# Performance work log

Hardware: AMD Instinct MI355X
Metric: run time of the kernel (lower is better)

The kernel has to match this reference:

```python
import jax, jax.numpy as jnp
import numpy as np
import math

L_, E_, H_, F_ = 6, 256, 8, 2048
NQ, B_, M_ = 300, 8, 1024

def _lin(x, w, b):
    return x @ w.T + b

def _ln(x, w, b):
    m = jnp.mean(x, -1, keepdims=True)
    v = jnp.var(x, -1, keepdims=True)
    return (x - m) / jnp.sqrt(v + 1e-5) * w + b

def _mha(q, k, v, iw, ib, ow, ob, H):
    # torch nn.MultiheadAttention, seq-first [L, B, E], packed in_proj
    E = q.shape[-1]; Dh = E // H
    wq, wk, wv = iw[:E], iw[E:2*E], iw[2*E:]
    bq, bk, bv = ib[:E], ib[E:2*E], ib[2*E:]
    qp = (_lin(q, wq, bq) * (Dh ** -0.5)).reshape(q.shape[0], q.shape[1], H, Dh)
    kp = _lin(k, wk, bk).reshape(k.shape[0], k.shape[1], H, Dh)
    vp = _lin(v, wv, bv).reshape(v.shape[0], v.shape[1], H, Dh)
    att = jax.nn.softmax(jnp.einsum('qbhd,kbhd->bhqk', qp, kp), axis=-1)
    o = jnp.einsum('bhqk,kbhd->qbhd', att, vp).reshape(q.shape[0], q.shape[1], E)
    return _lin(o, ow, ob)

def _sine4(pt):
    # pt: [nq, b, 4]; faithful to gen_sineembed_for_position4 incl. the
    # pos_w/pos_h re-use of the already-transformed pos_x/pos_y (original bug).
    dim_t = 10000.0 ** (2 * (jnp.arange(64) // 2).astype(jnp.float32) / 64)
    s = 2 * math.pi
    def iv(p):
        return jnp.stack([jnp.sin(p[:, :, 0::2]), jnp.cos(p[:, :, 1::2])], axis=3).reshape(p.shape[0], p.shape[1], -1)
    px = iv(pt[:, :, 0, None] * s / dim_t)
    py = iv(pt[:, :, 1, None] * s / dim_t)
    pw = iv(px)
    ph = iv(py)
    return jnp.concatenate([py, px, pw, ph], axis=2)


def setup_inputs() -> dict:
    key = jax.random.key(0)
    ks = iter(jax.random.split(key, 80))
    rn = lambda *s: jax.random.normal(next(ks), s, dtype=jnp.float32)
    rw = lambda *s: jax.random.normal(next(ks), s, dtype=jnp.float32) * 0.02
    d = dict(
        tgt=rn(NQ, B_, E_), memory=rn(M_, B_, E_), pos=rn(M_, B_, E_),
        query_pos=rn(NQ, B_, E_), box_embed=rn(NQ, B_, 4),
        sa_in_w=rw(L_, 3*E_, E_), sa_in_b=rw(L_, 3*E_), sa_out_w=rw(L_, E_, E_), sa_out_b=rw(L_, E_),
        ca_in_w=rw(L_, 3*E_, E_), ca_in_b=rw(L_, 3*E_), ca_out_w=rw(L_, E_, E_), ca_out_b=rw(L_, E_),
        ca_qpos_w=rw(E_, E_), ca_qpos_b=rw(E_),
        ca_kpos_w=rw(L_, E_, E_), ca_kpos_b=rw(L_, E_),
        ca_v_w=rw(L_, E_, E_), ca_v_b=rw(L_, E_),
        ca_kc_w=rw(L_, E_, E_), ca_kc_b=rw(L_, E_),
        ca_qs_w=rw(L_, E_, E_), ca_qs_b=rw(L_, E_),
        ca_vp_w=rw(L_, E_, E_), ca_vp_b=rw(L_, E_),
        lin1_w=rw(L_, F_, E_), lin1_b=rw(L_, F_), lin2_w=rw(L_, E_, F_), lin2_b=rw(L_, E_),
        lp1_w=rw(L_, F_, E_), lp1_b=rw(L_, F_), lp2_w=rw(L_, E_, F_), lp2_b=rw(L_, E_),
        norms_w=jnp.ones((L_, 6, E_), jnp.float32), norms_b=jnp.zeros((L_, 6, E_), jnp.float32),
        qs_w1=rw(E_, E_), qs_b1=rw(E_), qs_w2=rw(E_, E_), qs_b2=rw(E_),
        rh_w1=rw(E_, E_), rh_b1=rw(E_), rh_w2=rw(4, E_), rh_b2=rw(4),
        bo_w1=rw(L_, E_ // 2, 4), bo_b1=rw(L_, E_ // 2), bo_w2=rw(L_, 4, E_ // 2), bo_b2=rw(L_, 4),
    )
    return d


def _fwd(tgt, memory, pos, query_pos, box_embed, sa_in_w, sa_in_b, sa_out_w, sa_out_b,
         ca_in_w, ca_in_b, ca_out_w, ca_out_b, ca_qpos_w, ca_qpos_b, ca_kpos_w, ca_kpos_b,
         ca_v_w, ca_v_b, ca_kc_w, ca_kc_b, ca_qs_w, ca_qs_b, ca_vp_w, ca_vp_b,
         lin1_w, lin1_b, lin2_w, lin2_b, lp1_w, lp1_b, lp2_w, lp2_b, norms_w, norms_b,
         qs_w1, qs_b1, qs_w2, qs_b2, rh_w1, rh_b1, rh_w2, rh_b2, bo_w1, bo_b1, bo_w2, bo_b2):
    H = H_
    L = sa_in_w.shape[0]
    relu = jax.nn.relu
    # ref_point_head: MLP(d, d, 4, 2)
    rbs = _lin(relu(_lin(query_pos, rh_w1, rh_b1)), rh_w2, rh_b2)  # [nq,b,4]
    out = tgt
    for l in range(L):
        pt = 1.0 if l == 0 else _lin(relu(_lin(out, qs_w1, qs_b1)), qs_w2, qs_b2)
        rbs = rbs + _lin(relu(_lin(box_embed, bo_w1[l], bo_b1[l])), bo_w2[l], bo_b2[l])
        qse = _sine4(jax.nn.sigmoid(rbs)) * pt  # [nq,b,256]
        # self-attention (q = k = out + query_pos, v = out)
        q = out + query_pos
        t = _ln(out + _mha(q, q, out, sa_in_w[l], sa_in_b[l], sa_out_w[l], sa_out_b[l], H),
                norms_w[l, 0], norms_b[l, 0])
        # conditional cross-attention projections
        if l == 0:
            qc = t + _lin(query_pos, ca_qpos_w, ca_qpos_b)
            kk = memory + pos; v = memory; kpos = pos
        else:
            qc = t
            kpos = _lin(pos, ca_kpos_w[l], ca_kpos_b[l])
            v = _lin(memory, ca_v_w[l], ca_v_b[l])
            kk = _lin(memory, ca_kc_w[l], ca_kc_b[l])
        qse_p = _lin(qse, ca_qs_w[l], ca_qs_b[l])
        t2 = _mha(qc, kk, v, ca_in_w[l], ca_in_b[l], ca_out_w[l], ca_out_b[l], H)
        vpos = _lin(memory, ca_vp_w[l], ca_vp_b[l])
        t2p = _mha(qse_p, kpos, vpos, ca_in_w[l], ca_in_b[l], ca_out_w[l], ca_out_b[l], H)
        t2 = t2 + t2p
        # positional branch FFN
        tp = _ln(t + t2p, norms_w[l, 3], norms_b[l, 3])
        tp = _ln(tp + _lin(relu(_lin(tp, lp1_w[l], lp1_b[l])), lp2_w[l], lp2_b[l]),
                 norms_w[l, 4], norms_b[l, 4])
        # main branch FFN
        t = _ln(t + t2, norms_w[l, 1], norms_b[l, 1])
        t = _ln(t + _lin(relu(_lin(t, lin1_w[l], lin1_b[l])), lin2_w[l], lin2_b[l]),
                norms_w[l, 2], norms_b[l, 2])
        out = _ln(t + tp, norms_w[l, 5], norms_b[l, 5])
    return out[None]  # [1, nq, b, d] (return_intermediate=False -> unsqueeze(0))


def reference(tgt, memory, pos, query_pos, box_embed, sa_in_w, sa_in_b, sa_out_w, sa_out_b,
              ca_in_w, ca_in_b, ca_out_w, ca_out_b, ca_qpos_w, ca_qpos_b, ca_kpos_w, ca_kpos_b,
              ca_v_w, ca_v_b, ca_kc_w, ca_kc_b, ca_qs_w, ca_qs_b, ca_vp_w, ca_vp_b,
              lin1_w, lin1_b, lin2_w, lin2_b, lp1_w, lp1_b, lp2_w, lp2_b, norms_w, norms_b,
              qs_w1, qs_b1, qs_w2, qs_b2, rh_w1, rh_b1, rh_w2, rh_b2, bo_w1, bo_b1, bo_w2, bo_b2):
    return _fwd(tgt, memory, pos, query_pos, box_embed, sa_in_w, sa_in_b, sa_out_w, sa_out_b,
                ca_in_w, ca_in_b, ca_out_w, ca_out_b, ca_qpos_w, ca_qpos_b, ca_kpos_w, ca_kpos_b,
                ca_v_w, ca_v_b, ca_kc_w, ca_kc_b, ca_qs_w, ca_qs_b, ca_vp_w, ca_vp_b,
                lin1_w, lin1_b, lin2_w, lin2_b, lp1_w, lp1_b, lp2_w, lp2_b, norms_w, norms_b,
                qs_w1, qs_b1, qs_w2, qs_b2, rh_w1, rh_b1, rh_w2, rh_b2, bo_w1, bo_b1, bo_w2, bo_b2)
```

## Files before the change

### kernel.cpp

```cpp
#include <hip/hip_runtime.h>
#include <hip/hip_bf16.h>

#define NQq 300
#define BBb 8
#define MMm 1024
#define EEe 256
#define FFf 2048
#define LLl 6
#define RQ 2400
#define RM 8192
#define RPAD 2432

typedef unsigned short u16;
typedef short bf16x8 __attribute__((ext_vector_type(8)));
typedef float f32x4 __attribute__((ext_vector_type(4)));

__device__ __forceinline__ float u2f(u16 u){ return __uint_as_float(((unsigned)u)<<16); }
__device__ __forceinline__ u16 f2u(float v){
  __hip_bfloat16 h = __float2bfloat16(v);
  return *reinterpret_cast<u16*>(&h);
}
__device__ __forceinline__ int effdt(int t, int f){ return (t==0) ? 1 : ((t==1) ? 0 : (f?1:0)); }
__device__ __forceinline__ float ldd(const void* p, size_t i, int t, int f){
  if (t == 0) return ((const float*)p)[i];
  if (t == 1) return u2f(((const u16*)p)[i]);
  return f ? ((const float*)p)[i] : u2f(((const u16*)p)[i]);
}
__device__ __forceinline__ void ld8f(const void* p, size_t eoff, int e, float* o){
  if (e == 0) {
    uint4 v = *(const uint4*)((const u16*)p + eoff);
    u16 tmp[8]; *(uint4*)tmp = v;
#pragma unroll
    for (int u = 0; u < 8; ++u) o[u] = u2f(tmp[u]);
  } else {
    const float* q = (const float*)p + eoff;
    float4 v0 = ((const float4*)q)[0], v1 = ((const float4*)q)[1];
    o[0]=v0.x;o[1]=v0.y;o[2]=v0.z;o[3]=v0.w;o[4]=v1.x;o[5]=v1.y;o[6]=v1.z;o[7]=v1.w;
  }
}
__device__ __forceinline__ uint4 ld8pack(const void* p, size_t eoff, int e){
  if (e == 0) return *(const uint4*)((const u16*)p + eoff);
  float o[8]; ld8f(p, eoff, 1, o);
  u16 tmp[8];
#pragma unroll
  for (int u = 0; u < 8; ++u) tmp[u] = f2u(o[u]);
  return *(uint4*)tmp;
}

__global__ void k_flag_init(int* flag){ if (threadIdx.x==0 && blockIdx.x==0) *flag = 0; }
__global__ void k_detect(const u16* __restrict__ p, int n, int* flag){
  int hit = 0;
  for (int i = blockIdx.x*blockDim.x + threadIdx.x; i < n; i += gridDim.x*blockDim.x){
    u16 u = p[i];
    if ((u & 0x7F80u) == 0x7F80u) hit = 1;
  }
  if (hit) atomicOr(flag, 1);
}

__global__ void k_cvt_in(const void* __restrict__ s, float* __restrict__ d, int n,
                         const int* __restrict__ flag){
  int f = *flag;
  for (int i = blockIdx.x*blockDim.x + threadIdx.x; i < n; i += gridDim.x*blockDim.x)
    d[i] = ldd(s, i, 2, f);
}
__global__ void k_out_dual(const float* __restrict__ s, void* __restrict__ d, int n,
                           const int* __restrict__ flag){
  int f = *flag;
  for (int i = blockIdx.x*blockDim.x + threadIdx.x; i < n; i += gridDim.x*blockDim.x){
    if (f) ((float*)d)[i] = s[i];
    else   ((u16*)d)[i] = f2u(s[i]);
  }
}

struct CompW { const void* A[27]; size_t ao[27]; const void* B[27]; size_t bo[27]; u16* W[27]; };
__global__ __launch_bounds__(256) void k_compose_w(CompW cw, const int* __restrict__ flag){
  int f = *flag;
  int z = blockIdx.z;
  const void* A = cw.A[z]; size_t ao = cw.ao[z];
  const void* B = cw.B[z]; size_t bo = cw.bo[z];
  u16* Wo = cw.W[z];
  int ea = effdt(2,f), eb = ea;
  __shared__ __align__(16) u16 As[64*40];
  __shared__ __align__(16) u16 Bs[64*40];
  int bm = blockIdx.x*64, bn = blockIdx.y*64;
  int t = threadIdx.x;
  int lane = t & 63, wv = t >> 6;
  int wrow = (wv>>1)<<5, wcol = (wv&1)<<5;
  int quad = lane>>4, mr = lane&15;
  f32x4 a00 = {0.f,0.f,0.f,0.f}, a01 = a00, a10 = a00, a11 = a00;
  for (int k0 = 0; k0 < 256; k0 += 32){
    { int srow = t>>2, scg = (t&3)<<3;
      *(uint4*)&As[srow*40+scg] = ld8pack(A, ao + (size_t)(bm+srow)*256 + k0 + scg, ea); }
    { int kk = t>>3, c8 = (t&7)<<3;
      float o8[8]; ld8f(B, bo + (size_t)(k0+kk)*256 + bn + c8, eb, o8);
#pragma unroll
      for (int u = 0; u < 8; ++u) Bs[(c8+u)*40 + kk] = f2u(o8[u]); }
    __syncthreads();
    bf16x8 a0 = *(const bf16x8*)&As[(wrow+mr)*40+quad*8];
    bf16x8 a1 = *(const bf16x8*)&As[(wrow+16+mr)*40+quad*8];
    bf16x8 b0 = *(const bf16x8*)&Bs[(wcol+mr)*40+quad*8];
    bf16x8 b1 = *(const bf16x8*)&Bs[(wcol+16+mr)*40+quad*8];
    a00 = __builtin_amdgcn_mfma_f32_16x16x32_bf16(a0,b0,a00,0,0,0);
    a01 = __builtin_amdgcn_mfma_f32_16x16x32_bf16(a0,b1,a01,0,0,0);
    a10 = __builtin_amdgcn_mfma_f32_16x16x32_bf16(a1,b0,a10,0,0,0);
    a11 = __builtin_amdgcn_mfma_f32_16x16x32_bf16(a1,b1,a11,0,0,0);
    __syncthreads();
  }
  f32x4 av[4] = {a00,a01,a10,a11};
#pragma unroll
  for (int i = 0; i < 2; ++i)
#pragma unroll
  for (int j = 0; j < 2; ++j){
    f32x4 a = av[i*2+j];
    int col = bn + wcol + j*16 + mr;
#pragma unroll
    for (int r = 0; r < 4; ++r){
      int row = bm + wrow + i*16 + quad*4 + r;
      Wo[(size_t)row*256 + col] = f2u(a[r]);
    }
  }
}
struct CompB { const void* A[27]; size_t ao[27]; const void* b1[27]; size_t b1o[27];
               const void* b2[27]; size_t b2o[27]; u16* bo[27]; };
__global__ __launch_bounds__(256) void k_compose_b(CompB cb, const int* __restrict__ flag){
  int f = *flag;
  int z = blockIdx.x, o = threadIdx.x;
  float acc = 0.f;
  for (int j = 0; j < 256; ++j)
    acc += ldd(cb.A[z], cb.ao[z] + (size_t)o*256 + j, 2, f) * ldd(cb.b1[z], cb.b1o[z] + j, 2, f);
  cb.bo[z][o] = f2u(acc + ldd(cb.b2[z], cb.b2o[z] + o, 2, f));
}

__global__ __launch_bounds__(256) void k_gemm(
    const void* __restrict__ X1, size_t xo1, int xt1,
    const void* __restrict__ X2, size_t xo2, int xt2,
    const void* __restrict__ W1, size_t wo1, int wt1,
    const void* __restrict__ B1v, size_t bo1, int bt1,
    const void* __restrict__ W2, size_t wo2, int wt2,
    const void* __restrict__ B2v, size_t bo2, int bt2,
    void* __restrict__ Y, int yt, int ldy,
    int R, int K, int O, int Rsplit, int relu, const int* __restrict__ flag)
{
  __shared__ __align__(16) u16 As[64*40];
  __shared__ __align__(16) u16 Bs[64*40];
  int f = *flag;
  int bm = blockIdx.x*64, bn = blockIdx.y*64;
  bool second = (bm >= Rsplit);
  const void* W = second ? W2 : W1;  size_t wo = second ? wo2 : wo1;  int wt = second ? wt2 : wt1;
  const void* Bv = second ? B2v : B1v; size_t bo = second ? bo2 : bo1; int bt = second ? bt2 : bt1;
  int ex1 = effdt(xt1, f), ew = effdt(wt, f);
  int t = threadIdx.x;
  int srow = t >> 2, scg = (t & 3) << 3;
  int lane = t & 63, wv = t >> 6;
  int wrow = (wv >> 1) << 5, wcol = (wv & 1) << 5;
  int quad = lane >> 4, mr = lane & 15;
  f32x4 acc00 = {0.f,0.f,0.f,0.f}, acc01 = acc00, acc10 = acc00, acc11 = acc00;
  for (int k0 = 0; k0 < K; k0 += 32) {
    {
      int gr = bm + srow;
      uint4 v = {0u,0u,0u,0u};
      if (gr < R) {
        size_t e = xo1 + (size_t)gr*K + k0 + scg;
        if (xt2 < 0) v = ld8pack(X1, e, ex1);
        else {
          float a8[8], b8[8];
          ld8f(X1, e, ex1, a8);
          ld8f(X2, xo2 + (size_t)gr*K + k0 + scg, effdt(xt2,f), b8);
          u16 tmp[8];
#pragma unroll
          for (int u = 0; u < 8; ++u) tmp[u] = f2u(a8[u] + b8[u]);
          v = *(uint4*)tmp;
        }
      }
      *(uint4*)&As[srow*40 + scg] = v;
    }
    {
      int go = bn + srow;
      uint4 v = {0u,0u,0u,0u};
      if (go < O) v = ld8pack(W, wo + (size_t)go*K + k0 + scg, ew);
      *(uint4*)&Bs[srow*40 + scg] = v;
    }
    __syncthreads();
    bf16x8 a0 = *(const bf16x8*)&As[(wrow      + mr)*40 + quad*8];
    bf16x8 a1 = *(const bf16x8*)&As[(wrow + 16 + mr)*40 + quad*8];
    bf16x8 b0 = *(const bf16x8*)&Bs[(wcol      + mr)*40 + quad*8];
    bf16x8 b1 = *(const bf16x8*)&Bs[(wcol + 16 + mr)*40 + quad*8];
    acc00 = __builtin_amdgcn_mfma_f32_16x16x32_bf16(a0, b0, acc00, 0, 0, 0);
    acc01 = __builtin_amdgcn_mfma_f32_16x16x32_bf16(a0, b1, acc01, 0, 0, 0);
    acc10 = __builtin_amdgcn_mfma_f32_16x16x32_bf16(a1, b0, acc10, 0, 0, 0);
    acc11 = __builtin_amdgcn_mfma_f32_16x16x32_bf16(a1, b1, acc11, 0, 0, 0);
    __syncthreads();
  }
  f32x4 av[4] = {acc00, acc01, acc10, acc11};
#pragma unroll
  for (int i = 0; i < 2; ++i)
#pragma unroll
  for (int j = 0; j < 2; ++j) {
    f32x4 a = av[i*2 + j];
    int col = bn + wcol + j*16 + mr;
    if (col >= O) continue;
    float bv = ldd(Bv, bo + col, bt, f);
#pragma unroll
    for (int r = 0; r < 4; ++r) {
      int row = bm + wrow + i*16 + quad*4 + r;
      if (row >= R) continue;
      float v = a[r] + bv;
      if (relu) v = fmaxf(v, 0.f);
      if (yt == 0) ((float*)Y)[(size_t)row*ldy + col] = v;
      else         ((u16*)Y)[(size_t)row*ldy + col] = f2u(v);
    }
  }
}

__device__ __forceinline__ float blk_sum256(float v, float* red){
  for (int off = 32; off; off >>= 1) v += __shfl_down(v, off, 64);
  int lane = threadIdx.x & 63, w = threadIdx.x >> 6;
  if (lane == 0) red[w] = v;
  __syncthreads();
  v = red[0] + red[1] + red[2] + red[3];
  __syncthreads();
  return v;
}
__device__ __forceinline__ float ln_one(float x, size_t go, size_t bo,
    const void* gb, const void* bb, int f, float* red, int i){
  float m = blk_sum256(x, red) * (1.0f/256.0f);
  float d0 = x - m;
  float var = blk_sum256(d0*d0, red) * (1.0f/256.0f);
  float r = rsqrtf(var + 1e-5f);
  return d0 * r * ldd(gb, go + i, 2, f) + ldd(bb, bo + i, 2, f);
}
__global__ __launch_bounds__(256) void k_ln(
    const float* __restrict__ A, const float* __restrict__ Bp, const float* __restrict__ Cp,
    const void* __restrict__ gb, const void* __restrict__ bb, size_t o1,
    float* __restrict__ Y, const int* __restrict__ flag)
{
  __shared__ float red[4];
  int f = *flag;
  int row = blockIdx.x, i = threadIdx.x;
  size_t idx = (size_t)row*256 + i;
  float x = A[idx];
  if (Bp) x += Bp[idx];
  if (Cp) x += Cp[idx];
  Y[idx] = ln_one(x, o1, o1, gb, bb, f, red, i);
}
__global__ __launch_bounds__(256) void k_ln_pair(
    const float* __restrict__ A1, const float* __restrict__ B1, const float* __restrict__ C1,
    size_t o1, float* __restrict__ Y1,
    const float* __restrict__ A2, const float* __restrict__ B2,
    size_t o2, float* __restrict__ Y2,
    const void* __restrict__ gb, const void* __restrict__ bb, const int* __restrict__ flag)
{
  __shared__ float red[4];
  int f = *flag;
  int row = blockIdx.x, i = threadIdx.x;
  size_t idx = (size_t)row*256 + i;
  float x1 = A1[idx] + B1[idx];
  if (C1) x1 += C1[idx];
  float x2 = A2[idx] + B2[idx];
  float y1 = ln_one(x1, o1, o1, gb, bb, f, red, i);
  float y2 = ln_one(x2, o2, o2, gb, bb, f, red, i);
  Y1[idx] = y1;
  Y2[idx] = y2;
}

struct FP {
  const u16* Q[2]; int qs[2];
  const u16* K[2]; int ks[2];
  const u16* V[2]; int vs[2];
  u16* O[2];
};
__global__ __launch_bounds__(256) void k_flash_pair(FP fp, int NQr, int Nk, float scale)
{
  __shared__ __align__(16) u16 Qs[64*40];
  __shared__ __align__(16) u16 Ks[64*40];
  __shared__ __align__(16) u16 Vs[32*72];
  __shared__ __align__(16) u16 Ps[64*72];
  int z = blockIdx.z;
  const u16* Q = fp.Q[z]; int qstr = fp.qs[z];
  const u16* K = fp.K[z]; int kstr = fp.ks[z];
  const u16* V = fp.V[z]; int vstr = fp.vs[z];
  u16* O = fp.O[z];
  int t = threadIdx.x;
  int b = blockIdx.y >> 3, h = blockIdx.y & 7;
  int q0 = blockIdx.x * 64;
  int lane = t & 63, wv = t >> 6;
  int quad = lane >> 4, mr = lane & 15;
  {
    int qi = t >> 2, c8 = (t & 3) * 8;
    int qg = q0 + qi; if (qg >= NQr) qg = NQr - 1;
    *(uint4*)&Qs[qi*40 + c8] = *(const uint4*)(Q + ((size_t)qg*8 + b)*qstr + h*32 + c8);
  }
  f32x4 o0 = {0.f,0.f,0.f,0.f}, o1 = o0;
  float m_run[4], l_run[4];
#pragma unroll
  for (int r = 0; r < 4; ++r){ m_run[r] = -1e30f; l_run[r] = 0.f; }
  __syncthreads();

  for (int k0 = 0; k0 < Nk; k0 += 64) {
    {
      int ki = t >> 2, c8 = (t & 3)*8;
      int kg = k0 + ki;
      uint4 kv = {0u,0u,0u,0u}, vv = {0u,0u,0u,0u};
      if (kg < Nk) {
        kv = *(const uint4*)(K + ((size_t)kg*8 + b)*kstr + h*32 + c8);
        vv = *(const uint4*)(V + ((size_t)kg*8 + b)*vstr + h*32 + c8);
      }
      *(uint4*)&Ks[ki*40 + c8] = kv;
      u16 tmp[8]; *(uint4*)tmp = vv;
#pragma unroll
      for (int u = 0; u < 8; ++u) Vs[(c8+u)*72 + ki] = tmp[u];
    }
    __syncthreads();
    bf16x8 aq = *(const bf16x8*)&Qs[(wv*16 + mr)*40 + quad*8];
    f32x4 s[4];
#pragma unroll
    for (int j = 0; j < 4; ++j) {
      bf16x8 bk = *(const bf16x8*)&Ks[(j*16 + mr)*40 + quad*8];
      f32x4 zz = {0.f,0.f,0.f,0.f};
      s[j] = __builtin_amdgcn_mfma_f32_16x16x32_bf16(aq, bk, zz, 0, 0, 0);
      s[j] *= scale;
    }
    float alpha[4];
#pragma unroll
    for (int r = 0; r < 4; ++r) {
      float cm = -1e30f;
#pragma unroll
      for (int j = 0; j < 4; ++j) {
        int kg = k0 + j*16 + mr;
        cm = fmaxf(cm, (kg < Nk) ? s[j][r] : -1e30f);
      }
      for (int msk = 1; msk < 16; msk <<= 1)
        cm = fmaxf(cm, __shfl_xor(cm, msk, 64));
      float mn = fmaxf(m_run[r], cm);
      alpha[r] = __expf(m_run[r] - mn);
      m_run[r] = mn;
      float rsum = 0.f;
#pragma unroll
      for (int j = 0; j < 4; ++j) {
        int kg = k0 + j*16 + mr;
        float p = (kg < Nk) ? __expf(s[j][r] - mn) : 0.f;
        s[j][r] = p;
        rsum += p;
      }
      for (int msk = 1; msk < 16; msk <<= 1)
        rsum += __shfl_xor(rsum, msk, 64);
      l_run[r] = l_run[r]*alpha[r] + rsum;
    }
#pragma unroll
    for (int j = 0; j < 4; ++j)
#pragma unroll
      for (int r = 0; r < 4; ++r)
        Ps[(wv*16 + quad*4 + r)*72 + j*16 + mr] = f2u(s[j][r]);
    __syncthreads();
    f32x4 pv0 = {0.f,0.f,0.f,0.f}, pv1 = pv0;
#pragma unroll
    for (int st = 0; st < 2; ++st) {
      bf16x8 ap  = *(const bf16x8*)&Ps[(wv*16 + mr)*72 + st*32 + quad*8];
      bf16x8 bv0 = *(const bf16x8*)&Vs[(mr)*72      + st*32 + quad*8];
      bf16x8 bv1 = *(const bf16x8*)&Vs[(16 + mr)*72 + st*32 + quad*8];
      pv0 = __builtin_amdgcn_mfma_f32_16x16x32_bf16(ap, bv0, pv0, 0, 0, 0);
      pv1 = __builtin_amdgcn_mfma_f32_16x16x32_bf16(ap, bv1, pv1, 0, 0, 0);
    }
#pragma unroll
    for (int r = 0; r < 4; ++r) {
      o0[r] = o0[r]*alpha[r] + pv0[r];
      o1[r] = o1[r]*alpha[r] + pv1[r];
    }
    __syncthreads();
  }
#pragma unroll
  for (int r = 0; r < 4; ++r) {
    int qg = q0 + wv*16 + quad*4 + r;
    if (qg >= NQr) continue;
    float inv = 1.0f / l_run[r];
    u16* dst = O + ((size_t)qg*8 + b)*256 + h*32;
    dst[mr]      = f2u(o0[r]*inv);
    dst[16 + mr] = f2u(o1[r]*inv);
  }
}

__global__ __launch_bounds__(256) void k_boxsine(
    const void* __restrict__ box, const void* __restrict__ w1, size_t w1o,
    const void* __restrict__ b1v, size_t b1o,
    const void* __restrict__ w2, size_t w2o, const void* __restrict__ b2v, size_t b2o,
    float* __restrict__ RBS, const u16* __restrict__ pt, u16* __restrict__ qse,
    const int* __restrict__ flag)
{
  int f = *flag;
  int row = blockIdx.x, t = threadIdx.x;
  __shared__ float xs[4];
  __shared__ float hs[128];
  __shared__ float rb[4];
  if (t < 4) xs[t] = ldd(box, (size_t)row*4 + t, 2, f);
  __syncthreads();
  if (t < 128) {
    float acc = ldd(b1v, b1o + t, 2, f);
#pragma unroll
    for (int j = 0; j < 4; ++j) acc += ldd(w1, w1o + (size_t)t*4 + j, 2, f) * xs[j];
    hs[t] = fmaxf(acc, 0.f);
  }
  __syncthreads();
  if (t < 4) {
    float acc = ldd(b2v, b2o + t, 2, f);
    for (int j = 0; j < 128; ++j) acc += ldd(w2, w2o + (size_t)t*128 + j, 2, f) * hs[j];
    float nr = RBS[(size_t)row*4 + t] + acc;
    RBS[(size_t)row*4 + t] = nr;
    rb[t] = nr;
  }
  __syncthreads();
  int c = t >> 6, i = t & 63;
  float x = 1.f/(1.f + __expf(-rb[0]));
  float y = 1.f/(1.f + __expf(-rb[1]));
  int j = i >> 1;
  float dt = powf(10000.f, (float)(2*j)/64.f);
  const float s2pi = 6.283185307179586f;
  float base = (c == 0 || c == 3) ? y : x;
  float a = base * s2pi / dt;
  bool even = ((i & 1) == 0);
  float p1 = even ? sinf(a) : cosf(a);
  float v = (c <= 1) ? p1 : (even ? sinf(p1) : cosf(p1));
  if (pt) v *= u2f(pt[(size_t)row*256 + t]);
  qse[(size_t)row*256 + t] = f2u(v);
}

extern "C" void kernel_launch(void* const* d_in, const int* in_sizes, int n_in,
                              void* d_out, int out_size, void* d_ws, size_t ws_size,
                              hipStream_t stream) {
  (void)in_sizes; (void)n_in; (void)out_size; (void)ws_size;

  int* FLAG = (int*)d_ws;
  float* f32p = (float*)((char*)d_ws + 16);
  size_t fo = 0;
  auto AF = [&](size_t n){ float* p = f32p + fo; fo += n; return p; };
  float* OUT = AF(614400);
  float* T   = AF((size_t)RPAD*256);
  float* TP  = AF((size_t)RPAD*256);
  float* T2  = AF(614400);
  float* T2P = AF(614400);
  float* Q1  = AF((size_t)2*RPAD*256);
  float* RBS = AF(9600);
  u16* u16p = (u16*)(f32p + fo);
  size_t uo = 0;
  auto AU = [&](size_t n){ u16* p = u16p + uo; uo += (n + 7) & ~(size_t)7; return p; };
  u16* QSE  = AU(614400);
  u16* QC   = AU(614400);
  u16* AO   = AU(2*614400);
  u16* PT   = AU(614400);
  u16* QB   = AU(2*614400);
  u16* QKB  = AU(1228800);
  u16* KVV  = AU((size_t)RM*768);
  u16* KPOS = AU((size_t)RM*256);
  u16* KSPARE = AU((size_t)RM*256);
  u16* HID  = KVV;
  u16* SAV  = KPOS;
  u16* QPW  = AU(6*65536);  u16* QPB  = AU(6*256);
  u16* KVVW = AU(5*196608); u16* KVVB = AU(5*768);
  u16* KPW  = AU(5*65536);  u16* KPB  = AU(5*256);
  u16* VP0W = AU(65536);    u16* VP0B = AU(256);
  (void)KSPARE;

  k_flag_init<<<1,64,0,stream>>>(FLAG);
  k_detect<<<256,256,0,stream>>>((const u16*)d_in[1], 262144, FLAG);
  k_cvt_in<<<600,256,0,stream>>>(d_in[0], OUT, RQ*EEe, FLAG);

  {
    CompW cw; CompB cb; int nz = 0;
    auto addc = [&](int ia, size_t ao, int ib, size_t bo_, u16* W,
                    int ib1, size_t b1o, int ib2, size_t b2o, u16* bo){
      cw.A[nz]=d_in[ia]; cw.ao[nz]=ao; cw.B[nz]=d_in[ib]; cw.bo[nz]=bo_; cw.W[nz]=W;
      cb.A[nz]=d_in[ia]; cb.ao[nz]=ao; cb.b1[nz]=d_in[ib1]; cb.b1o[nz]=b1o;
      cb.b2[nz]=d_in[ib2]; cb.b2o[nz]=b2o; cb.bo[nz]=bo; ++nz;
    };
    for (int l = 0; l < 6; ++l)
      addc(9,(size_t)l*196608, 21,(size_t)l*65536, QPW+(size_t)l*65536,
           22,(size_t)l*256, 10,(size_t)l*768, QPB+(size_t)l*256);
    for (int l = 1; l < 6; ++l) {
      size_t wk = (size_t)l*196608 + 65536, wv = (size_t)l*196608 + 131072;
      u16* WS = KVVW + (size_t)(l-1)*196608;
      u16* BS = KVVB + (size_t)(l-1)*768;
      addc(9,wk, 19,(size_t)l*65536, WS,        20,(size_t)l*256, 10,(size_t)l*768+256, BS);
      addc(9,wv, 17,(size_t)l*65536, WS+65536,  18,(size_t)l*256, 10,(size_t)l*768+512, BS+256);
      addc(9,wv, 23,(size_t)l*65536, WS+131072, 24,(size_t)l*256, 10,(size_t)l*768+512, BS+512);
      addc(9,wk, 15,(size_t)l*65536, KPW+(size_t)(l-1)*65536,
           16,(size_t)l*256, 10,(size_t)l*768+256, KPB+(size_t)(l-1)*256);
    }
    addc(9,131072, 23,0, VP0W, 24,0, 10,512, VP0B);
    k_compose_w<<<dim3(4,4,27),256,0,stream>>>(cw, FLAG);
    k_compose_b<<<27,256,0,stream>>>(cb, FLAG);
  }

  struct P { const void* p; size_t o; int t; };
  auto GEMM = [&](P X1, P X2, P W1, P B1, P W2, P B2, void* Y, int yt, int ldy,
                  int R, int K, int O, int Rsplit, int relu){
    dim3 g((R+63)/64, (O+63)/64);
    k_gemm<<<g,256,0,stream>>>(X1.p,X1.o,X1.t, X2.p,X2.o,X2.t, W1.p,W1.o,W1.t,
                               B1.p,B1.o,B1.t, W2.p,W2.o,W2.t, B2.p,B2.o,B2.t,
                               Y,yt,ldy,R,K,O,Rsplit,relu,FLAG);
  };
  P NONE = {nullptr, 0, -1};
  auto RAW = [&](int i, size_t o){ P p = {d_in[i], o, 2}; return p; };
  auto WS1 = [&](const u16* q){ P p = {q, 0, 1}; return p; };
  auto WS0 = [&](const float* q){ P p = {q, 0, 0}; return p; };
  auto G1 = [&](P X, P W, P B, void* Y, int yt, int ldy, int R, int K, int O, int relu){
    GEMM(X, NONE, W, B, W, B, Y, yt, ldy, R, K, O, R+64, relu);
  };
  auto LN1k = [&](const float* A, const float* Bp, const float* Cp, int l, int j, float* Y){
    size_t o1 = ((size_t)l*6 + j)*EEe;
    k_ln<<<RQ,256,0,stream>>>(A,Bp,Cp, d_in[33], d_in[34], o1, Y, FLAG);
  };
  const float rs = 0.17677669529663687f;

  G1(RAW(3,0), RAW(39,0), RAW(40,0), QC, 1, 256, RQ, 256, 256, 1);
  G1(WS1(QC),  RAW(41,0), RAW(42,0), RBS, 0, 4,  RQ, 256, 4,   0);

  for (int l = 0; l < LLl; ++l) {
    size_t sw = (size_t)l*196608, sb = (size_t)l*768;
    if (l > 0) {
      G1(WS0(OUT), RAW(35,0), RAW(36,0), QC, 1, 256, RQ, 256, 256, 1);
      G1(WS1(QC),  RAW(37,0), RAW(38,0), PT, 1, 256, RQ, 256, 256, 0);
    }
    k_boxsine<<<RQ,256,0,stream>>>(d_in[4], d_in[43],(size_t)l*512, d_in[44],(size_t)l*128,
                                   d_in[45],(size_t)l*512, d_in[46],(size_t)l*4,
                                   RBS, l > 0 ? PT : (const u16*)nullptr, QSE, FLAG);

    GEMM(WS0(OUT), RAW(3,0), RAW(5,sw), RAW(6,sb), NONE, NONE,
         QKB, 1, 512, RQ, 256, 512, RQ+64, 0);
    G1(WS0(OUT), RAW(5,sw+131072), RAW(6,sb+512), SAV, 1, 256, RQ, 256, 256, 0);
    {
      FP fp = {};
      fp.Q[0]=QKB; fp.qs[0]=512; fp.K[0]=QKB+256; fp.ks[0]=512;
      fp.V[0]=SAV; fp.vs[0]=256; fp.O[0]=AO;
      k_flash_pair<<<dim3(5,64,1),256,0,stream>>>(fp, NQq, NQq, rs);
    }
    G1(WS1(AO), RAW(7,(size_t)l*65536), RAW(8,(size_t)l*256), Q1, 0, 256, RQ, 256, 256, 0);
    LN1k(OUT, Q1, nullptr, l, 0, T);

    if (l == 0) {
      GEMM(RAW(1,0), RAW(2,0), RAW(9,sw+65536), RAW(10,sb+256), NONE, NONE,
           KVV, 1, 768, RM, 256, 256, RM+64, 0);
      G1(RAW(1,0), RAW(9,sw+131072), RAW(10,sb+512), KVV+256, 1, 768, RM, 256, 256, 0);
      G1(RAW(1,0), WS1(VP0W), WS1(VP0B), KVV+512, 1, 768, RM, 256, 256, 0);
      G1(RAW(2,0), RAW(9,sw+65536), RAW(10,sb+256), KPOS, 1, 256, RM, 256, 256, 0);
    } else {
      G1(RAW(1,0), WS1(KVVW+(size_t)(l-1)*196608), WS1(KVVB+(size_t)(l-1)*768),
         KVV, 1, 768, RM, 256, 768, 0);
      G1(RAW(2,0), WS1(KPW+(size_t)(l-1)*65536), WS1(KPB+(size_t)(l-1)*256),
         KPOS, 1, 256, RM, 256, 256, 0);
    }

    if (l == 0) {
      G1(RAW(3,0), RAW(13,0), RAW(14,0), Q1, 0, 256, RQ, 256, 256, 0);
      GEMM(WS0(T), WS0(Q1), RAW(9,sw), RAW(10,sb), NONE, NONE,
           QB, 1, 256, RQ, 256, 256, RQ+64, 0);
    } else {
      G1(WS0(T), RAW(9,sw), RAW(10,sb), QB, 1, 256, RQ, 256, 256, 0);
    }
    G1(WS1(QSE), WS1(QPW+(size_t)l*65536), WS1(QPB+(size_t)l*256),
       QB+614400, 1, 256, RQ, 256, 256, 0);

    {
      FP fp = {};
      fp.Q[0]=QB;        fp.qs[0]=256; fp.K[0]=KVV;     fp.ks[0]=768;
      fp.V[0]=KVV+256;   fp.vs[0]=768; fp.O[0]=AO;
      fp.Q[1]=QB+614400; fp.qs[1]=256; fp.K[1]=KPOS;    fp.ks[1]=256;
      fp.V[1]=KVV+512;   fp.vs[1]=768; fp.O[1]=AO+614400;
      k_flash_pair<<<dim3(5,64,2),256,0,stream>>>(fp, NQq, MMm, rs);
    }
    G1(WS1(AO), RAW(11,(size_t)l*65536), RAW(12,(size_t)l*256),
       T2, 0, 256, 2*RQ, 256, 256, 0);

    k_ln_pair<<<RQ,256,0,stream>>>(T, T2, T2P, ((size_t)l*6+1)*EEe, T,
                                   T, T2P, ((size_t)l*6+3)*EEe, TP,
                                   d_in[33], d_in[34], FLAG);

    GEMM(WS0(T), NONE, RAW(25,(size_t)l*524288), RAW(26,(size_t)l*2048),
         RAW(29,(size_t)l*524288), RAW(30,(size_t)l*2048),
         HID, 1, 2048, 2*RPAD, 256, 2048, RPAD, 1);
    GEMM(WS1(HID), NONE, RAW(27,(size_t)l*524288), RAW(28,(size_t)l*256),
         RAW(31,(size_t)l*524288), RAW(32,(size_t)l*256),
         Q1, 0, 256, 2*RPAD, 2048, 256, RPAD, 0);

    k_ln_pair<<<RQ,256,0,stream>>>(T, Q1, nullptr, ((size_t)l*6+2)*EEe, T,
                                   TP, Q1 + (size_t)RPAD*256, ((size_t)l*6+4)*EEe, TP,
                                   d_in[33], d_in[34], FLAG);

    LN1k(T, TP, nullptr, l, 5, OUT);
  }

  k_out_dual<<<600,256,0,stream>>>(OUT, d_out, RQ*EEe, FLAG);
}
```

Before: 2.329 ms.

## Split-K the FFN down-projection GEMM and widen the GEMM K-step to 64

The GEMM kernel now stages 64-wide K slices in shared memory per iteration, issuing two MFMA sub-steps per barrier pair instead of one, which halves the synchronisation count. It also gains split-K support through blockIdx.z. The K=2048 FFN second GEMM is split into four K chunks that write partial sums to a new workspace buffer, and a k_sum4 kernel adds them into Q1. The aim is more parallelism for that 2048-deep GEMM, at the cost of extra partial-sum traffic, one more launch and doubled shared-memory tiles.

```diff
diff --git a/kernel.cpp b/kernel.cpp
--- a/kernel.cpp
+++ b/kernel.cpp
@@ -69,6 +69,17 @@
   for (int i = blockIdx.x*blockDim.x + threadIdx.x; i < n; i += gridDim.x*blockDim.x){
     if (f) ((float*)d)[i] = s[i];
     else   ((u16*)d)[i] = f2u(s[i]);
+  }
+}
+__global__ void k_sum4(const float* __restrict__ P, size_t s, float* __restrict__ Y, int n4){
+  for (int i = blockIdx.x*blockDim.x + threadIdx.x; i < n4; i += gridDim.x*blockDim.x){
+    float4 a = ((const float4*)P)[i];
+    float4 b = ((const float4*)(P + s))[i];
+    float4 c = ((const float4*)(P + 2*s))[i];
+    float4 d = ((const float4*)(P + 3*s))[i];
+    float4 o; o.x=a.x+b.x+c.x+d.x; o.y=a.y+b.y+c.y+d.y;
+    o.z=a.z+b.z+c.z+d.z; o.w=a.w+b.w+c.w+d.w;
+    ((float4*)Y)[i] = o;
   }
 }
 
@@ -138,13 +149,17 @@
     const void* __restrict__ B1v, size_t bo1, int bt1,
     const void* __restrict__ W2, size_t wo2, int wt2,
     const void* __restrict__ B2v, size_t bo2, int bt2,
-    void* __restrict__ Y, int yt, int ldy,
-    int R, int K, int O, int Rsplit, int relu, const int* __restrict__ flag)
+    void* __restrict__ Y, int yt, int ldy, size_t zstride,
+    int R, int K, int O, int Rsplit, int relu, int kchunk,
+    const int* __restrict__ flag)
 {
-  __shared__ __align__(16) u16 As[64*40];
-  __shared__ __align__(16) u16 Bs[64*40];
+  __shared__ __align__(16) u16 As[64*72];
+  __shared__ __align__(16) u16 Bs[64*72];
   int f = *flag;
   int bm = blockIdx.x*64, bn = blockIdx.y*64;
+  int z = blockIdx.z;
+  int kbeg = z * kchunk;
+  int kend = kbeg + kchunk; if (kend > K) kend = K;
   bool second = (bm >= Rsplit);
   const void* W = second ? W2 : W1;  size_t wo = second ? wo2 : wo1;  int wt = second ? wt2 : wt1;
   const void* Bv = second ? B2v : B1v; size_t bo = second ? bo2 : bo1; int bt = second ? bt2 : bt1;
@@ -155,42 +170,60 @@
   int wrow = (wv >> 1) << 5, wcol = (wv & 1) << 5;
   int quad = lane >> 4, mr = lane & 15;
   f32x4 acc00 = {0.f,0.f,0.f,0.f}, acc01 = acc00, acc10 = acc00, acc11 = acc00;
-  for (int k0 = 0; k0 < K; k0 += 32) {
+  for (int k0 = kbeg; k0 < kend; k0 += 64) {
     {
       int gr = bm + srow;
-      uint4 v = {0u,0u,0u,0u};
+      uint4 v0 = {0u,0u,0u,0u}, v1 = v0;
       if (gr < R) {
         size_t e = xo1 + (size_t)gr*K + k0 + scg;
-        if (xt2 < 0) v = ld8pack(X1, e, ex1);
-        else {
-          float a8[8], b8[8];
-          ld8f(X1, e, ex1, a8);
-          ld8f(X2, xo2 + (size_t)gr*K + k0 + scg, effdt(xt2,f), b8);
-          u16 tmp[8];
+        if (xt2 < 0) {
+          v0 = ld8pack(X1, e, ex1);
+          v1 = ld8pack(X1, e + 32, ex1);
+        } else {
+          int ex2 = effdt(xt2, f);
+          size_t e2 = xo2 + (size_t)gr*K + k0 + scg;
+          float a8[8], b8[8]; u16 tmp[8];
+          ld8f(X1, e, ex1, a8); ld8f(X2, e2, ex2, b8);
 #pragma unroll
           for (int u = 0; u < 8; ++u) tmp[u] = f2u(a8[u] + b8[u]);
-          v = *(uint4*)tmp;
+          v0 = *(uint4*)tmp;
+          ld8f(X1, e + 32, ex1, a8); ld8f(X2, e2 + 32, ex2, b8);
+#pragma unroll
+          for (int u = 0; u < 8; ++u) tmp[u] = f2u(a8[u] + b8[u]);
+          v1 = *(uint4*)tmp;
         }
       }
-      *(uint4*)&As[srow*40 + scg] = v;
+      *(uint4*)&As[srow*72 + scg]      = v0;
+      *(uint4*)&As[srow*72 + 32 + scg] = v1;
     }
     {
       int go = bn + srow;
-      uint4 v = {0u,0u,0u,0u};
-      if (go < O) v = ld8pack(W, wo + (size_t)go*K + k0 + scg, ew);
-      *(uint4*)&Bs[srow*40 + scg] = v;
+      uint4 v0 = {0u,0u,0u,0u}, v1 = v0;
+      if (go < O) {
+        size_t e = wo + (size_t)go*K + k0 + scg;
+        v0 = ld8pack(W, e, ew);
+        v1 = ld8pack(W, e + 32, ew);
+      }
+      *(uint4*)&Bs[srow*72 + scg]      = v0;
+      *(uint4*)&Bs[srow*72 + 32 + scg] = v1;
     }
     __syncthreads();
-    bf16x8 a0 = *(const bf16x8*)&As[(wrow      + mr)*40 + quad*8];
-    bf16x8 a1 = *(const bf16x8*)&As[(wrow + 16 + mr)*40 + quad*8];
-    bf16x8 b0 = *(const bf16x8*)&Bs[(wcol      + mr)*40 + quad*8];
-    bf16x8 b1 = *(const bf16x8*)&Bs[(wcol + 16 + mr)*40 + quad*8];
-    acc00 = __builtin_amdgcn_mfma_f32_16x16x32_bf16(a0, b0, acc00, 0, 0, 0);
-    acc01 = __builtin_amdgcn_mfma_f32_16x16x32_bf16(a0, b1, acc01, 0, 0, 0);
-    acc10 = __builtin_amdgcn_mfma_f32_16x16x32_bf16(a1, b0, acc10, 0, 0, 0);
-    acc11 = __builtin_amdgcn_mfma_f32_16x16x32_bf16(a1, b1, acc11, 0, 0, 0);
+#pragma unroll
+    for (int ks = 0; ks < 2; ++ks) {
+      int kb = ks*32 + quad*8;
+      bf16x8 a0 = *(const bf16x8*)&As[(wrow      + mr)*72 + kb];
+      bf16x8 a1 = *(const bf16x8*)&As[(wrow + 16 + mr)*72 + kb];
+      bf16x8 b0 = *(const bf16x8*)&Bs[(wcol      + mr)*72 + kb];
+      bf16x8 b1 = *(const bf16x8*)&Bs[(wcol + 16 + mr)*72 + kb];
+      acc00 = __builtin_amdgcn_mfma_f32_16x16x32_bf16(a0, b0, acc00, 0, 0, 0);
+      acc01 = __builtin_amdgcn_mfma_f32_16x16x32_bf16(a0, b1, acc01, 0, 0, 0);
+      acc10 = __builtin_amdgcn_mfma_f32_16x16x32_bf16(a1, b0, acc10, 0, 0, 0);
+      acc11 = __builtin_amdgcn_mfma_f32_16x16x32_bf16(a1, b1, acc11, 0, 0, 0);
+    }
     __syncthreads();
   }
+  float* Yf = (float*)Y + z*zstride;
+  u16*   Yu = (u16*)Y + z*zstride;
   f32x4 av[4] = {acc00, acc01, acc10, acc11};
 #pragma unroll
   for (int i = 0; i < 2; ++i)
@@ -199,15 +232,15 @@
     f32x4 a = av[i*2 + j];
     int col = bn + wcol + j*16 + mr;
     if (col >= O) continue;
-    float bv = ldd(Bv, bo + col, bt, f);
+    float bv = (z == 0) ? ldd(Bv, bo + col, bt, f) : 0.f;
 #pragma unroll
     for (int r = 0; r < 4; ++r) {
       int row = bm + wrow + i*16 + quad*4 + r;
       if (row >= R) continue;
       float v = a[r] + bv;
       if (relu) v = fmaxf(v, 0.f);
-      if (yt == 0) ((float*)Y)[(size_t)row*ldy + col] = v;
-      else         ((u16*)Y)[(size_t)row*ldy + col] = f2u(v);
+      if (yt == 0) Yf[(size_t)row*ldy + col] = v;
+      else         Yu[(size_t)row*ldy + col] = f2u(v);
     }
   }
 }
@@ -438,6 +471,7 @@
   float* T2  = AF(614400);
   float* T2P = AF(614400);
   float* Q1  = AF((size_t)2*RPAD*256);
+  float* PART= AF((size_t)4*2*RPAD*256);
   float* RBS = AF(9600);
   u16* u16p = (u16*)(f32p + fo);
   size_t uo = 0;
@@ -491,18 +525,21 @@
 
   struct P { const void* p; size_t o; int t; };
   auto GEMM = [&](P X1, P X2, P W1, P B1, P W2, P B2, void* Y, int yt, int ldy,
-                  int R, int K, int O, int Rsplit, int relu){
-    dim3 g((R+63)/64, (O+63)/64);
+                  int R, int K, int O, int Rsplit, int relu, int kc, int gz, size_t zs){
+    dim3 g((R+63)/64, (O+63)/64, gz);
     k_gemm<<<g,256,0,stream>>>(X1.p,X1.o,X1.t, X2.p,X2.o,X2.t, W1.p,W1.o,W1.t,
                                B1.p,B1.o,B1.t, W2.p,W2.o,W2.t, B2.p,B2.o,B2.t,
-                               Y,yt,ldy,R,K,O,Rsplit,relu,FLAG);
+                               Y,yt,ldy,zs,R,K,O,Rsplit,relu,kc,FLAG);
   };
   P NONE = {nullptr, 0, -1};
   auto RAW = [&](int i, size_t o){ P p = {d_in[i], o, 2}; return p; };
   auto WS1 = [&](const u16* q){ P p = {q, 0, 1}; return p; };
   auto WS0 = [&](const float* q){ P p = {q, 0, 0}; return p; };
   auto G1 = [&](P X, P W, P B, void* Y, int yt, int ldy, int R, int K, int O, int relu){
-    GEMM(X, NONE, W, B, W, B, Y, yt, ldy, R, K, O, R+64, relu);
+    GEMM(X, NONE, W, B, W, B, Y, yt, ldy, R, K, O, R+64, relu, K, 1, 0);
+  };
+  auto G2 = [&](P X, P X2, P W, P B, void* Y, int yt, int ldy, int R, int K, int O){
+    GEMM(X, X2, W, B, W, B, Y, yt, ldy, R, K, O, R+64, 0, K, 1, 0);
   };
   auto LN1k = [&](const float* A, const float* Bp, const float* Cp, int l, int j, float* Y){
     size_t o1 = ((size_t)l*6 + j)*EEe;
@@ -523,8 +560,7 @@
                                    d_in[45],(size_t)l*512, d_in[46],(size_t)l*4,
                                    RBS, l > 0 ? PT : (const u16*)nullptr, QSE, FLAG);
 
-    GEMM(WS0(OUT), RAW(3,0), RAW(5,sw), RAW(6,sb), NONE, NONE,
-         QKB, 1, 512, RQ, 256, 512, RQ+64, 0);
+    G2(WS0(OUT), RAW(3,0), RAW(5,sw), RAW(6,sb), QKB, 1, 512, RQ, 256, 512);
     G1(WS0(OUT), RAW(5,sw+131072), RAW(6,sb+512), SAV, 1, 256, RQ, 256, 256, 0);
     {
       FP fp = {};
@@ -536,8 +572,7 @@
     LN1k(OUT, Q1, nullptr, l, 0, T);
 
     if (l == 0) {
-      GEMM(RAW(1,0), RAW(2,0), RAW(9,sw+65536), RAW(10,sb+256), NONE, NONE,
-           KVV, 1, 768, RM, 256, 256, RM+64, 0);
+      G2(RAW(1,0), RAW(2,0), RAW(9,sw+65536), RAW(10,sb+256), KVV, 1, 768, RM, 256, 256);
       G1(RAW(1,0), RAW(9,sw+131072), RAW(10,sb+512), KVV+256, 1, 768, RM, 256, 256, 0);
       G1(RAW(1,0), WS1(VP0W), WS1(VP0B), KVV+512, 1, 768, RM, 256, 256, 0);
       G1(RAW(2,0), RAW(9,sw+65536), RAW(10,sb+256), KPOS, 1, 256, RM, 256, 256, 0);
@@ -550,8 +585,7 @@
 
     if (l == 0) {
       G1(RAW(3,0), RAW(13,0), RAW(14,0), Q1, 0, 256, RQ, 256, 256, 0);
-      GEMM(WS0(T), WS0(Q1), RAW(9,sw), RAW(10,sb), NONE, NONE,
-           QB, 1, 256, RQ, 256, 256, RQ+64, 0);
+      G2(WS0(T), WS0(Q1), RAW(9,sw), RAW(10,sb), QB, 1, 256, RQ, 256, 256);
     } else {
       G1(WS0(T), RAW(9,sw), RAW(10,sb), QB, 1, 256, RQ, 256, 256, 0);
     }
@@ -575,10 +609,11 @@
 
     GEMM(WS0(T), NONE, RAW(25,(size_t)l*524288), RAW(26,(size_t)l*2048),
          RAW(29,(size_t)l*524288), RAW(30,(size_t)l*2048),
-         HID, 1, 2048, 2*RPAD, 256, 2048, RPAD, 1);
+         HID, 1, 2048, 2*RPAD, 256, 2048, RPAD, 1, 256, 1, 0);
     GEMM(WS1(HID), NONE, RAW(27,(size_t)l*524288), RAW(28,(size_t)l*256),
          RAW(31,(size_t)l*524288), RAW(32,(size_t)l*256),
-         Q1, 0, 256, 2*RPAD, 2048, 256, RPAD, 0);
+         PART, 0, 256, 2*RPAD, 2048, 256, RPAD, 0, 512, 4, (size_t)2*RPAD*256);
+    k_sum4<<<1216,256,0,stream>>>(PART, (size_t)2*RPAD*256, Q1, (2*RPAD*256)/4);
 
     k_ln_pair<<<RQ,256,0,stream>>>(T, Q1, nullptr, ((size_t)l*6+2)*EEe, T,
                                    TP, Q1 + (size_t)RPAD*256, ((size_t)l*6+4)*EEe, TP,
```

New measurement: 2.028 ms. 1.15x faster.
